# Optimization experiments

Measured on AMD Instinct MI355X. Metric: run time of the kernel, lower is better.

Reference implementation:

```python
import jax, jax.numpy as jnp
import numpy as np

HEADS = 16
DIM_HEAD = 64
SCALE = DIM_HEAD ** -0.5
MASK_VALUE = -jnp.finfo(jnp.float32).max


def setup_inputs() -> dict:
    key = jax.random.key(0)
    ks = jax.random.split(key, 6)
    b, n, dim = 2, 2048, 1024
    mem_len = 2048
    inner = HEADS * DIM_HEAD  # 1024
    return {
        "x": jax.random.normal(ks[0], (b, n, dim), jnp.float32),
        "mem_k": jax.random.normal(ks[1], (b, mem_len, inner), jnp.float32),
        "mem_v": jax.random.normal(ks[2], (b, mem_len, inner), jnp.float32),
        "pos_bias": jax.random.normal(ks[3], (HEADS, n, mem_len + n), jnp.float32) * 0.02,
        "Wq": jax.random.normal(ks[4], (dim, inner), jnp.float32) * (dim ** -0.5),
        "Wkv": jax.random.normal(ks[5], (dim, 2 * inner), jnp.float32) * (dim ** -0.5),
    }


def reference(x, mem_k, mem_v, pos_bias, Wq, Wkv):
    b, n, _ = x.shape
    # projections (note: original module returns before applying to_out)
    q = (x @ Wq) * SCALE                      # [b, n, h*d]
    k, v = jnp.split(x @ Wkv, 2, axis=-1)     # each [b, n, h*d]
    k = jnp.concatenate((mem_k, k), axis=1)   # [b, j, h*d]
    v = jnp.concatenate((mem_v, v), axis=1)

    def split_heads(t):
        return t.reshape(t.shape[0], t.shape[1], HEADS, DIM_HEAD).transpose(0, 2, 1, 3)

    q, k, v = map(split_heads, (q, k, v))     # [b, h, i/j, d]
    sim = jnp.einsum('bhid,bhjd->bhij', q, k)
    sim = sim + pos_bias[None]                # broadcast over batch
    i, j = sim.shape[-2:]
    # causal mask: triu with offset j - i + 1 is masked out
    causal_mask = jnp.triu(jnp.ones((i, j), dtype=bool), k=j - i + 1)
    sim = jnp.where(causal_mask[None, None], MASK_VALUE, sim)
    attn = jax.nn.softmax(sim, axis=-1)
    out = jnp.einsum('bhij,bhjd->bhid', attn, v)     # [b, h, i, d]
    out = out.transpose(0, 2, 1, 3).reshape(b, n, HEADS * DIM_HEAD)
    return out
```

## Files before the change

### kernel.cpp

```cpp
#include <hip/hip_runtime.h>
#include <hip/hip_bf16.h>
#include <cstdint>

#define B_     2
#define N_     2048
#define DIM_   1024
#define H_     16
#define DH_    64
#define MEM_   2048
#define JT_    4096
#define INNER_ 1024
#define SCALE_ 0.125f

typedef float f32x4 __attribute__((ext_vector_type(4)));
typedef short s16x8 __attribute__((ext_vector_type(8)));
typedef short s16x4 __attribute__((ext_vector_type(4)));

__device__ __forceinline__ short bf16_of(float f) {
    __hip_bfloat16 h = __float2bfloat16(f);
    return *(short*)&h;
}

__device__ __forceinline__ void gload16(const void* g, short* l) {
    __builtin_amdgcn_global_load_lds(
        (const __attribute__((address_space(1))) unsigned int*)g,
        (__attribute__((address_space(3))) unsigned int*)l, 16, 0, 0);
}

__global__ __launch_bounds__(256) void cast_x(
    const float* __restrict__ x, short* __restrict__ xb)
{
    const int total4 = B_ * N_ * DIM_ / 4;
    for (int idx = blockIdx.x * blockDim.x + threadIdx.x; idx < total4;
         idx += gridDim.x * blockDim.x) {
        float4 v = ((const float4*)x)[idx];
        s16x4 o;
        o[0] = bf16_of(v.x); o[1] = bf16_of(v.y);
        o[2] = bf16_of(v.z); o[3] = bf16_of(v.w);
        *(s16x4*)&xb[idx * 4] = o;
    }
}

__global__ __launch_bounds__(256) void cast_w(
    const float* __restrict__ Wq, const float* __restrict__ Wkv,
    short* __restrict__ Wt)
{
    const int kt = blockIdx.x;
    const int nt = blockIdx.y;
    __shared__ float tile[64][65];
    const int t = threadIdx.x;
    const int r = t >> 2, s4 = (t & 3) * 16;

    const int n0 = nt * 64;
    const float* src;
    int ldn, nc0;
    if (n0 < 1024) { src = Wq;  ldn = 1024; nc0 = n0; }
    else           { src = Wkv; ldn = 2048; nc0 = n0 - 1024; }
    const float scale = (n0 < 1024) ? SCALE_ : 1.0f;

#pragma unroll
    for (int kq = 0; kq < 4; ++kq) {
        float4 v = *(const float4*)&src[(size_t)(kt * 64 + r) * ldn + nc0 + s4 + kq * 4];
        tile[s4 + kq * 4 + 0][r] = v.x;
        tile[s4 + kq * 4 + 1][r] = v.y;
        tile[s4 + kq * 4 + 2][r] = v.z;
        tile[s4 + kq * 4 + 3][r] = v.w;
    }
    __syncthreads();
    short ov[16];
#pragma unroll
    for (int e = 0; e < 16; ++e) ov[e] = bf16_of(tile[r][s4 + e] * scale);
    short* dst = &Wt[(size_t)(n0 + r) * 1024 + kt * 64 + s4];
    *(s16x8*)&dst[0] = *(s16x8*)&ov[0];
    *(s16x8*)&dst[8] = *(s16x8*)&ov[8];
}

#define PLDC 152

__global__ __launch_bounds__(256) void mfma_proj(
    const short* __restrict__ Wt, const short* __restrict__ xb,
    short* __restrict__ qbuf, short* __restrict__ kbuf, short* __restrict__ vtbuf)
{
    const int bc = blockIdx.x;
    const int bi = blockIdx.y;
    const int tid = threadIdx.x;
    const int w = tid >> 6, lane = tid & 63, g = lane >> 4, li = lane & 15;
    const int wr = w >> 1, wc = w & 1;

    __shared__ short smem[128 * PLDC];
    short* A_lds = smem;
    short* B_lds = smem + 8192;

    f32x4 acc[4][4];
#pragma unroll
    for (int m = 0; m < 4; ++m)
#pragma unroll
        for (int n = 0; n < 4; ++n) acc[m][n] = f32x4{0.f, 0.f, 0.f, 0.f};

    const size_t arow0 = (size_t)bc * 128;
    const size_t brow0 = (size_t)bi * 128;

    for (int t = 0; t < 16; ++t) {
        __syncthreads();
#pragma unroll
        for (int u = 0; u < 4; ++u) {
            const int c = (w * 4 + u) * 64 + lane;
            const int row = c >> 3, q = c & 7;
            const int qs = q ^ (row & 7);
            gload16(&Wt[(arow0 + row) * 1024 + t * 64 + qs * 8],
                    &A_lds[(w * 4 + u) * 512 + lane * 8]);
            gload16(&xb[(brow0 + row) * 1024 + t * 64 + qs * 8],
                    &B_lds[(w * 4 + u) * 512 + lane * 8]);
        }
        __syncthreads();
#pragma unroll
        for (int kc = 0; kc < 2; ++kc) {
            s16x8 af[4], bf[4];
#pragma unroll
            for (int mt = 0; mt < 4; ++mt) {
                const int row = wr * 64 + mt * 16 + li;
                af[mt] = *(const s16x8*)&A_lds[row * 64 + ((kc * 4 + g) ^ (row & 7)) * 8];
            }
#pragma unroll
            for (int nt = 0; nt < 4; ++nt) {
                const int row = wc * 64 + nt * 16 + li;
                bf[nt] = *(const s16x8*)&B_lds[row * 64 + ((kc * 4 + g) ^ (row & 7)) * 8];
            }
#pragma unroll
            for (int mt = 0; mt < 4; ++mt)
#pragma unroll
                for (int nt = 0; nt < 4; ++nt)
                    acc[mt][nt] = __builtin_amdgcn_mfma_f32_16x16x32_bf16(af[mt], bf[nt], acc[mt][nt], 0, 0, 0);
        }
    }

    __syncthreads();
    const int c0 = bc * 128;
    const int i0g = bi * 128;
    const int b = i0g >> 11;
    const int ii0 = i0g & 2047;

    if (c0 < 2048) {
#pragma unroll
        for (int mt = 0; mt < 4; ++mt)
#pragma unroll
            for (int nt = 0; nt < 4; ++nt) {
                const int i_l = wc * 64 + nt * 16 + li;
                const int c_l = wr * 64 + mt * 16 + g * 4;
                s16x4 v4;
                v4[0] = bf16_of(acc[mt][nt][0]);
                v4[1] = bf16_of(acc[mt][nt][1]);
                v4[2] = bf16_of(acc[mt][nt][2]);
                v4[3] = bf16_of(acc[mt][nt][3]);
                *(s16x4*)&smem[i_l * PLDC + c_l] = v4;
            }
        __syncthreads();
        const bool isq = (c0 < 1024);
#pragma unroll
        for (int u = 0; u < 8; ++u) {
            const int ch = tid + u * 256;
            const int i_l = ch >> 4, seg = ch & 15;
            s16x8 v = *(const s16x8*)&smem[i_l * PLDC + seg * 8];
            const int cg = c0 + seg * 8;
            const int h = (cg >> 6) & 15;
            const int d = cg & 63;
            if (isq)
                *(s16x8*)&qbuf[(((size_t)(b * H_ + h)) * N_ + ii0 + i_l) * DH_ + d] = v;
            else
                *(s16x8*)&kbuf[(((size_t)(b * H_ + h)) * JT_ + MEM_ + ii0 + i_l) * DH_ + d] = v;
        }
    } else {
#pragma unroll
        for (int mt = 0; mt < 4; ++mt)
#pragma unroll
            for (int nt = 0; nt < 4; ++nt) {
                const int i_l = wc * 64 + nt * 16 + li;
                const int c_b = wr * 64 + mt * 16 + g * 4;
#pragma unroll
                for (int r = 0; r < 4; ++r)
                    smem[(c_b + r) * PLDC + i_l] = bf16_of(acc[mt][nt][r]);
            }
        __syncthreads();
#pragma unroll
        for (int u = 0; u < 8; ++u) {
            const int ch = tid + u * 256;
            const int c_l = ch >> 4, seg = ch & 15;
            s16x8 v = *(const s16x8*)&smem[c_l * PLDC + seg * 8];
            const int cv = c0 + c_l - 2048;
            const int h = cv >> 6, d = cv & 63;
            *(s16x8*)&vtbuf[(((size_t)(b * H_ + h)) * DH_ + d) * JT_ + MEM_ + ii0 + seg * 8] = v;
        }
    }
}

__global__ __launch_bounds__(256) void copymem_k(
    const float* __restrict__ mem_k, short* __restrict__ kbuf)
{
    const int total4 = B_ * MEM_ * INNER_ / 4;
    for (int idx = blockIdx.x * blockDim.x + threadIdx.x; idx < total4;
         idx += gridDim.x * blockDim.x) {
        const int flat = idx * 4;
        const int c = flat & 1023;
        const int j = (flat >> 10) & 2047;
        const int b = flat >> 21;
        const int h = c >> 6, d = c & 63;
        float4 v = ((const float4*)mem_k)[idx];
        s16x4 o;
        o[0] = bf16_of(v.x); o[1] = bf16_of(v.y);
        o[2] = bf16_of(v.z); o[3] = bf16_of(v.w);
        *(s16x4*)&kbuf[(((size_t)(b * H_ + h)) * JT_ + j) * DH_ + d] = o;
    }
}

__global__ __launch_bounds__(256) void transpose_memv(
    const float* __restrict__ mem_v, short* __restrict__ vtbuf)
{
    const int jt = blockIdx.x, h = blockIdx.y, b = blockIdx.z;
    const int j0 = jt * 64;
    __shared__ float tile[64][65];
    const int t = threadIdx.x;
    const int r = t >> 2, s4 = (t & 3) * 16;
#pragma unroll
    for (int k = 0; k < 4; ++k) {
        float4 v = *(const float4*)&mem_v[((size_t)(b * MEM_ + j0 + r)) * INNER_ + h * DH_ + s4 + k * 4];
        tile[s4 + k * 4 + 0][r] = v.x;
        tile[s4 + k * 4 + 1][r] = v.y;
        tile[s4 + k * 4 + 2][r] = v.z;
        tile[s4 + k * 4 + 3][r] = v.w;
    }
    __syncthreads();
    short ov[16];
#pragma unroll
    for (int e = 0; e < 16; ++e) ov[e] = bf16_of(tile[r][s4 + e]);
    short* dst = &vtbuf[((size_t)((b * H_ + h) * DH_ + r)) * JT_ + j0 + s4];
    *(s16x8*)&dst[0] = *(s16x8*)&ov[0];
    *(s16x8*)&dst[8] = *(s16x8*)&ov[8];
}

#define LPP 72

__global__ __launch_bounds__(256) void attn_flash(
    const short* __restrict__ qbuf, const short* __restrict__ kbuf,
    const short* __restrict__ vtbuf, const float* __restrict__ pos_bias,
    float* __restrict__ out)
{
    const int lid = blockIdx.x;
    const int k_  = lid & 255;
    const int hi  = lid >> 8;
    const int h   = (k_ & 7) | (((k_ >> 3) & 1) << 3);
    const int b   = (k_ >> 4) & 1;
    const int ztl = k_ >> 5;
    const int zt  = hi ? (15 - ztl) : ztl;
    const int i0  = zt * 128;

    const int tid = threadIdx.x;
    const int w = tid >> 6, lane = tid & 63, g = lane >> 4, li = lane & 15;

    __shared__ short K_lds[2][64 * 64];
    __shared__ short VT_lds[2][64 * 64];
    __shared__ short P_lds[4][32 * LPP];

    const size_t bh = b * H_ + h;
    const short* kg  = kbuf  + bh * (size_t)JT_ * DH_;
    const short* vtg = vtbuf + bh * (size_t)DH_ * JT_;
    const float* pb  = pos_bias + (size_t)h * N_ * JT_;

    const int qw = i0 + w * 32;

    s16x8 aq[2][2];
#pragma unroll
    for (int mt = 0; mt < 2; ++mt)
#pragma unroll
        for (int kc = 0; kc < 2; ++kc)
            aq[mt][kc] = *(const s16x8*)&qbuf[(bh * N_ + qw + mt * 16 + li) * DH_ + kc * 32 + g * 8];

    f32x4 o[2][4];
    float m_run[2], l_run[2];
#pragma unroll
    for (int mt = 0; mt < 2; ++mt) {
#pragma unroll
        for (int dt = 0; dt < 4; ++dt) o[mt][dt] = f32x4{0.f, 0.f, 0.f, 0.f};
        m_run[mt] = -3.0e38f; l_run[mt] = 0.f;
    }

    const int ntiles = 34 + 2 * zt;

    #define STAGE(bufi, j0s)                                                   \
    {                                                                          \
        _Pragma("unroll")                                                      \
        for (int u = 0; u < 2; ++u) {                                          \
            const int c = u * 256 + tid;                                       \
            const int row = c >> 3, q = c & 7;                                 \
            const int qs = q ^ (row & 7);                                      \
            gload16(&kg[(size_t)((j0s) + row) * DH_ + qs * 8],                 \
                    &K_lds[bufi][c * 8]);                                      \
            gload16(&vtg[(size_t)row * JT_ + (j0s) + qs * 8],                  \
                    &VT_lds[bufi][c * 8]);                                     \
        }                                                                      \
    }

    f32x4 bnext[2][4];
    #define LOADB(j0s)                                                         \
    {                                                                          \
        _Pragma("unroll")                                                      \
        for (int mt = 0; mt < 2; ++mt)                                         \
        _Pragma("unroll")                                                      \
        for (int nt = 0; nt < 4; ++nt)                                         \
            bnext[mt][nt] = *(const f32x4*)&pb[(size_t)(qw + mt * 16 + li) * JT_ + (j0s) + nt * 16 + g * 4]; \
    }

    STAGE(0, 0);
    LOADB(0);
    __syncthreads();

    for (int t = 0; t < ntiles; ++t) {
        const int cur = t & 1;
        const int j0 = t * 64;

        if (t + 1 < ntiles) STAGE(cur ^ 1, j0 + 64);

        f32x4 sacc[2][4];
#pragma unroll
        for (int mt = 0; mt < 2; ++mt)
#pragma unroll
            for (int nt = 0; nt < 4; ++nt) sacc[mt][nt] = bnext[mt][nt];

        if (t + 1 < ntiles) LOADB(j0 + 64);

        __builtin_amdgcn_s_setprio(1);
#pragma unroll
        for (int kc = 0; kc < 2; ++kc)
#pragma unroll
            for (int nt = 0; nt < 4; ++nt) {
                s16x8 bk = *(const s16x8*)&K_lds[cur][(nt * 16 + li) * 64 + ((kc * 4 + g) ^ (li & 7)) * 8];
                sacc[0][nt] = __builtin_amdgcn_mfma_f32_16x16x32_bf16(bk, aq[0][kc], sacc[0][nt], 0, 0, 0);
                sacc[1][nt] = __builtin_amdgcn_mfma_f32_16x16x32_bf16(bk, aq[1][kc], sacc[1][nt], 0, 0, 0);
            }
        __builtin_amdgcn_s_setprio(0);

#pragma unroll
        for (int mt = 0; mt < 2; ++mt) {
            const int q = qw + mt * 16 + li;
            if (j0 + 63 > MEM_ + qw + mt * 16) {
#pragma unroll
                for (int nt = 0; nt < 4; ++nt)
#pragma unroll
                    for (int r = 0; r < 4; ++r) {
                        const int jg = j0 + nt * 16 + g * 4 + r;
                        if (jg > MEM_ + q) sacc[mt][nt][r] = -1e30f;
                    }
            }
            float t0 = fmaxf(fmaxf(sacc[mt][0][0], sacc[mt][0][1]), fmaxf(sacc[mt][0][2], sacc[mt][0][3]));
            float t1 = fmaxf(fmaxf(sacc[mt][1][0], sacc[mt][1][1]), fmaxf(sacc[mt][1][2], sacc[mt][1][3]));
            float t2 = fmaxf(fmaxf(sacc[mt][2][0], sacc[mt][2][1]), fmaxf(sacc[mt][2][2], sacc[mt][2][3]));
            float t3 = fmaxf(fmaxf(sacc[mt][3][0], sacc[mt][3][1]), fmaxf(sacc[mt][3][2], sacc[mt][3][3]));
            float tm = fmaxf(fmaxf(t0, t1), fmaxf(t2, t3));
            tm = fmaxf(tm, __shfl_xor(tm, 16));
            tm = fmaxf(tm, __shfl_xor(tm, 32));
            const float m_new = fmaxf(m_run[mt], tm);
            const float sc = __expf(m_run[mt] - m_new);
            m_run[mt] = m_new;

#pragma unroll
            for (int nt = 0; nt < 4; ++nt)
#pragma unroll
                for (int r = 0; r < 4; ++r)
                    sacc[mt][nt][r] = __expf(sacc[mt][nt][r] - m_new);

            float s0 = (sacc[mt][0][0] + sacc[mt][0][1]) + (sacc[mt][0][2] + sacc[mt][0][3]);
            float s1 = (sacc[mt][1][0] + sacc[mt][1][1]) + (sacc[mt][1][2] + sacc[mt][1][3]);
            float s2 = (sacc[mt][2][0] + sacc[mt][2][1]) + (sacc[mt][2][2] + sacc[mt][2][3]);
            float s3 = (sacc[mt][3][0] + sacc[mt][3][1]) + (sacc[mt][3][2] + sacc[mt][3][3]);
            float ts = (s0 + s1) + (s2 + s3);
            ts += __shfl_xor(ts, 16);
            ts += __shfl_xor(ts, 32);
            l_run[mt] = l_run[mt] * sc + ts;
#pragma unroll
            for (int dt = 0; dt < 4; ++dt) o[mt][dt] *= sc;

#pragma unroll
            for (int nt = 0; nt < 4; ++nt) {
                s16x4 pk;
                pk[0] = bf16_of(sacc[mt][nt][0]);
                pk[1] = bf16_of(sacc[mt][nt][1]);
                pk[2] = bf16_of(sacc[mt][nt][2]);
                pk[3] = bf16_of(sacc[mt][nt][3]);
                *(s16x4*)&P_lds[w][(mt * 16 + li) * LPP + nt * 16 + g * 4] = pk;
            }
        }

        __builtin_amdgcn_s_setprio(1);
#pragma unroll
        for (int kc = 0; kc < 2; ++kc) {
            s16x8 pf[2];
#pragma unroll
            for (int mt = 0; mt < 2; ++mt) {
                s16x4 plo = *(const s16x4*)&P_lds[w][(mt * 16 + li) * LPP + kc * 32 + g * 8];
                s16x4 phi = *(const s16x4*)&P_lds[w][(mt * 16 + li) * LPP + kc * 32 + g * 8 + 4];
#pragma unroll
                for (int e = 0; e < 4; ++e) { pf[mt][e] = plo[e]; pf[mt][4 + e] = phi[e]; }
            }
#pragma unroll
            for (int dt = 0; dt < 4; ++dt) {
                s16x8 bv = *(const s16x8*)&VT_lds[cur][(dt * 16 + li) * 64 + ((kc * 4 + g) ^ (li & 7)) * 8];
                o[0][dt] = __builtin_amdgcn_mfma_f32_16x16x32_bf16(bv, pf[0], o[0][dt], 0, 0, 0);
                o[1][dt] = __builtin_amdgcn_mfma_f32_16x16x32_bf16(bv, pf[1], o[1][dt], 0, 0, 0);
            }
        }
        __builtin_amdgcn_s_setprio(0);

        __syncthreads();
    }
    #undef STAGE
    #undef LOADB

#pragma unroll
    for (int mt = 0; mt < 2; ++mt) {
        const float rinv = 1.0f / l_run[mt];
        const int q = qw + mt * 16 + li;
#pragma unroll
        for (int dt = 0; dt < 4; ++dt) {
            f32x4 ov = o[mt][dt] * rinv;
            *(f32x4*)&out[((size_t)(b * N_ + q)) * INNER_ + h * DH_ + dt * 16 + g * 4] = ov;
        }
    }
}

extern "C" void kernel_launch(void* const* d_in, const int* in_sizes, int n_in,
                              void* d_out, int out_size, void* d_ws, size_t ws_size,
                              hipStream_t stream)
{
    const float* x        = (const float*)d_in[0];
    const float* mem_k    = (const float*)d_in[1];
    const float* mem_v    = (const float*)d_in[2];
    const float* pos_bias = (const float*)d_in[3];
    const float* Wq       = (const float*)d_in[4];
    const float* Wkv      = (const float*)d_in[5];
    float* out = (float*)d_out;

    char* ws = (char*)d_ws;
    short* qbuf  = (short*)(ws);
    short* kbuf  = (short*)(ws + (8u << 20));
    short* vtbuf = (short*)(ws + (24u << 20));
    short* xb    = (short*)(ws + (40u << 20));
    short* Wt    = (short*)(ws + (48u << 20));

    cast_x<<<2048, 256, 0, stream>>>(x, xb);
    cast_w<<<dim3(16, 48), 256, 0, stream>>>(Wq, Wkv, Wt);
    copymem_k<<<2048, 256, 0, stream>>>(mem_k, kbuf);
    transpose_memv<<<dim3(32, H_, B_), 256, 0, stream>>>(mem_v, vtbuf);

    mfma_proj<<<dim3(24, 32), 256, 0, stream>>>(Wt, xb, qbuf, kbuf, vtbuf);

    attn_flash<<<512, 256, 0, stream>>>(qbuf, kbuf, vtbuf, pos_bias, out);
}
```

Before: 263.6 us.

## Drop LDS staging of K/V and read fragments directly from global memory

Removes the double-buffered LDS staging of K and V^T tiles and has each warp load its MFMA operands straight from global memory (relying on L1/L2). Blocks are remapped so each block covers 64 query rows, with warps split across the two batches and half-tiles of queries, giving finer causal tile counts. This cuts LDS traffic and the block-wide sync, but each warp now issues its own uncoalesced global K/V loads with no sharing across warps, exposing global latency inside the MFMA loop.

```diff
diff --git a/kernel.cpp b/kernel.cpp
--- a/kernel.cpp
+++ b/kernel.cpp
@@ -248,25 +248,22 @@
     const int k_  = lid & 255;
     const int hi  = lid >> 8;
     const int h   = (k_ & 7) | (((k_ >> 3) & 1) << 3);
-    const int b   = (k_ >> 4) & 1;
-    const int ztl = k_ >> 5;
-    const int zt  = hi ? (15 - ztl) : ztl;
-    const int i0  = zt * 128;
+    const int zql = k_ >> 4;
+    const int zq  = hi ? (31 - zql) : zql;
+    const int i0  = zq * 64;
 
     const int tid = threadIdx.x;
     const int w = tid >> 6, lane = tid & 63, g = lane >> 4, li = lane & 15;
-
-    __shared__ short K_lds[2][64 * 64];
-    __shared__ short VT_lds[2][64 * 64];
+    const int b  = w & 1;
+    const int qw = i0 + (w >> 1) * 32;
+
     __shared__ short P_lds[4][32 * LPP];
 
-    const size_t bh = b * H_ + h;
+    const size_t bh = (size_t)(b * H_ + h);
     const short* kg  = kbuf  + bh * (size_t)JT_ * DH_;
     const short* vtg = vtbuf + bh * (size_t)DH_ * JT_;
     const float* pb  = pos_bias + (size_t)h * N_ * JT_;
 
-    const int qw = i0 + w * 32;
-
     s16x8 aq[2][2];
 #pragma unroll
     for (int mt = 0; mt < 2; ++mt)
@@ -283,21 +280,7 @@
         m_run[mt] = -3.0e38f; l_run[mt] = 0.f;
     }
 
-    const int ntiles = 34 + 2 * zt;
-
-    #define STAGE(bufi, j0s)                                                   \
-    {                                                                          \
-        _Pragma("unroll")                                                      \
-        for (int u = 0; u < 2; ++u) {                                          \
-            const int c = u * 256 + tid;                                       \
-            const int row = c >> 3, q = c & 7;                                 \
-            const int qs = q ^ (row & 7);                                      \
-            gload16(&kg[(size_t)((j0s) + row) * DH_ + qs * 8],                 \
-                    &K_lds[bufi][c * 8]);                                      \
-            gload16(&vtg[(size_t)row * JT_ + (j0s) + qs * 8],                  \
-                    &VT_lds[bufi][c * 8]);                                     \
-        }                                                                      \
-    }
+    const int ntiles = 33 + zq;
 
     f32x4 bnext[2][4];
     #define LOADB(j0s)                                                         \
@@ -309,16 +292,13 @@
             bnext[mt][nt] = *(const f32x4*)&pb[(size_t)(qw + mt * 16 + li) * JT_ + (j0s) + nt * 16 + g * 4]; \
     }
 
-    STAGE(0, 0);
     LOADB(0);
-    __syncthreads();
 
     for (int t = 0; t < ntiles; ++t) {
-        const int cur = t & 1;
+        __builtin_amdgcn_s_barrier();
+
         const int j0 = t * 64;
 
-        if (t + 1 < ntiles) STAGE(cur ^ 1, j0 + 64);
-
         f32x4 sacc[2][4];
 #pragma unroll
         for (int mt = 0; mt < 2; ++mt)
@@ -332,7 +312,7 @@
         for (int kc = 0; kc < 2; ++kc)
 #pragma unroll
             for (int nt = 0; nt < 4; ++nt) {
-                s16x8 bk = *(const s16x8*)&K_lds[cur][(nt * 16 + li) * 64 + ((kc * 4 + g) ^ (li & 7)) * 8];
+                s16x8 bk = *(const s16x8*)&kg[(size_t)(j0 + nt * 16 + li) * DH_ + kc * 32 + g * 8];
                 sacc[0][nt] = __builtin_amdgcn_mfma_f32_16x16x32_bf16(bk, aq[0][kc], sacc[0][nt], 0, 0, 0);
                 sacc[1][nt] = __builtin_amdgcn_mfma_f32_16x16x32_bf16(bk, aq[1][kc], sacc[1][nt], 0, 0, 0);
             }
@@ -402,16 +382,13 @@
             }
 #pragma unroll
             for (int dt = 0; dt < 4; ++dt) {
-                s16x8 bv = *(const s16x8*)&VT_lds[cur][(dt * 16 + li) * 64 + ((kc * 4 + g) ^ (li & 7)) * 8];
+                s16x8 bv = *(const s16x8*)&vtg[(size_t)(dt * 16 + li) * JT_ + j0 + kc * 32 + g * 8];
                 o[0][dt] = __builtin_amdgcn_mfma_f32_16x16x32_bf16(bv, pf[0], o[0][dt], 0, 0, 0);
                 o[1][dt] = __builtin_amdgcn_mfma_f32_16x16x32_bf16(bv, pf[1], o[1][dt], 0, 0, 0);
             }
         }
         __builtin_amdgcn_s_setprio(0);
-
-        __syncthreads();
-    }
-    #undef STAGE
+    }
     #undef LOADB
 
 #pragma unroll
```

After: 416.3 us. 57.9% more time.

## Split attention block into 8 waves of 16 query rows each

Applied to the files above, without the earlier changes.

The flash-attention kernel moves from 4 waves each owning 32 query rows to 8 waves each owning 16 rows, launched with 512 threads per block. Each wave now holds half the accumulators and bias registers, and every thread issues one global-to-LDS load per stage instead of two. The aim is more waves in flight to hide the pos_bias global-load latency and the softmax work. In exchange each K/V LDS fragment read feeds only one MFMA instead of two, so LDS traffic per MFMA doubles, and barrier synchronisation now spans more waves.

```diff
diff --git a/kernel.cpp b/kernel.cpp
--- a/kernel.cpp
+++ b/kernel.cpp
@@ -239,7 +239,7 @@
 
 #define LPP 72
 
-__global__ __launch_bounds__(256) void attn_flash(
+__global__ __launch_bounds__(512) void attn_flash(
     const short* __restrict__ qbuf, const short* __restrict__ kbuf,
     const short* __restrict__ vtbuf, const float* __restrict__ pos_bias,
     float* __restrict__ out)
@@ -258,55 +258,44 @@
 
     __shared__ short K_lds[2][64 * 64];
     __shared__ short VT_lds[2][64 * 64];
-    __shared__ short P_lds[4][32 * LPP];
-
-    const size_t bh = b * H_ + h;
+    __shared__ short P_lds[8][16 * LPP];
+
+    const size_t bh = (size_t)(b * H_ + h);
     const short* kg  = kbuf  + bh * (size_t)JT_ * DH_;
     const short* vtg = vtbuf + bh * (size_t)DH_ * JT_;
     const float* pb  = pos_bias + (size_t)h * N_ * JT_;
 
-    const int qw = i0 + w * 32;
-
-    s16x8 aq[2][2];
-#pragma unroll
-    for (int mt = 0; mt < 2; ++mt)
-#pragma unroll
-        for (int kc = 0; kc < 2; ++kc)
-            aq[mt][kc] = *(const s16x8*)&qbuf[(bh * N_ + qw + mt * 16 + li) * DH_ + kc * 32 + g * 8];
-
-    f32x4 o[2][4];
-    float m_run[2], l_run[2];
-#pragma unroll
-    for (int mt = 0; mt < 2; ++mt) {
-#pragma unroll
-        for (int dt = 0; dt < 4; ++dt) o[mt][dt] = f32x4{0.f, 0.f, 0.f, 0.f};
-        m_run[mt] = -3.0e38f; l_run[mt] = 0.f;
-    }
+    const int qw = i0 + w * 16;
+
+    s16x8 aq[2];
+#pragma unroll
+    for (int kc = 0; kc < 2; ++kc)
+        aq[kc] = *(const s16x8*)&qbuf[(bh * N_ + qw + li) * DH_ + kc * 32 + g * 8];
+
+    f32x4 o[4];
+    float m_run = -3.0e38f, l_run = 0.f;
+#pragma unroll
+    for (int dt = 0; dt < 4; ++dt) o[dt] = f32x4{0.f, 0.f, 0.f, 0.f};
 
     const int ntiles = 34 + 2 * zt;
 
     #define STAGE(bufi, j0s)                                                   \
     {                                                                          \
-        _Pragma("unroll")                                                      \
-        for (int u = 0; u < 2; ++u) {                                          \
-            const int c = u * 256 + tid;                                       \
-            const int row = c >> 3, q = c & 7;                                 \
-            const int qs = q ^ (row & 7);                                      \
-            gload16(&kg[(size_t)((j0s) + row) * DH_ + qs * 8],                 \
-                    &K_lds[bufi][c * 8]);                                      \
-            gload16(&vtg[(size_t)row * JT_ + (j0s) + qs * 8],                  \
-                    &VT_lds[bufi][c * 8]);                                     \
-        }                                                                      \
-    }
-
-    f32x4 bnext[2][4];
+        const int c = tid;                                                     \
+        const int row = c >> 3, q = c & 7;                                     \
+        const int qs = q ^ (row & 7);                                          \
+        gload16(&kg[(size_t)((j0s) + row) * DH_ + qs * 8],                     \
+                &K_lds[bufi][c * 8]);                                          \
+        gload16(&vtg[(size_t)row * JT_ + (j0s) + qs * 8],                      \
+                &VT_lds[bufi][c * 8]);                                         \
+    }
+
+    f32x4 bnext[4];
     #define LOADB(j0s)                                                         \
     {                                                                          \
         _Pragma("unroll")                                                      \
-        for (int mt = 0; mt < 2; ++mt)                                         \
-        _Pragma("unroll")                                                      \
         for (int nt = 0; nt < 4; ++nt)                                         \
-            bnext[mt][nt] = *(const f32x4*)&pb[(size_t)(qw + mt * 16 + li) * JT_ + (j0s) + nt * 16 + g * 4]; \
+            bnext[nt] = *(const f32x4*)&pb[(size_t)(qw + li) * JT_ + (j0s) + nt * 16 + g * 4]; \
     }
 
     STAGE(0, 0);
@@ -316,16 +305,15 @@
     for (int t = 0; t < ntiles; ++t) {
         const int cur = t & 1;
         const int j0 = t * 64;
-
-        if (t + 1 < ntiles) STAGE(cur ^ 1, j0 + 64);
-
-        f32x4 sacc[2][4];
-#pragma unroll
-        for (int mt = 0; mt < 2; ++mt)
-#pragma unroll
-            for (int nt = 0; nt < 4; ++nt) sacc[mt][nt] = bnext[mt][nt];
-
-        if (t + 1 < ntiles) LOADB(j0 + 64);
+        const bool more = (t + 1 < ntiles);
+
+        if (more) STAGE(cur ^ 1, j0 + 64);
+
+        f32x4 sacc[4];
+#pragma unroll
+        for (int nt = 0; nt < 4; ++nt) sacc[nt] = bnext[nt];
+
+        if (more) LOADB(j0 + 64);
 
         __builtin_amdgcn_s_setprio(1);
 #pragma unroll
@@ -333,78 +321,67 @@
 #pragma unroll
             for (int nt = 0; nt < 4; ++nt) {
                 s16x8 bk = *(const s16x8*)&K_lds[cur][(nt * 16 + li) * 64 + ((kc * 4 + g) ^ (li & 7)) * 8];
-                sacc[0][nt] = __builtin_amdgcn_mfma_f32_16x16x32_bf16(bk, aq[0][kc], sacc[0][nt], 0, 0, 0);
-                sacc[1][nt] = __builtin_amdgcn_mfma_f32_16x16x32_bf16(bk, aq[1][kc], sacc[1][nt], 0, 0, 0);
+                sacc[nt] = __builtin_amdgcn_mfma_f32_16x16x32_bf16(bk, aq[kc], sacc[nt], 0, 0, 0);
             }
         __builtin_amdgcn_s_setprio(0);
 
-#pragma unroll
-        for (int mt = 0; mt < 2; ++mt) {
-            const int q = qw + mt * 16 + li;
-            if (j0 + 63 > MEM_ + qw + mt * 16) {
-#pragma unroll
-                for (int nt = 0; nt < 4; ++nt)
-#pragma unroll
-                    for (int r = 0; r < 4; ++r) {
-                        const int jg = j0 + nt * 16 + g * 4 + r;
-                        if (jg > MEM_ + q) sacc[mt][nt][r] = -1e30f;
-                    }
-            }
-            float t0 = fmaxf(fmaxf(sacc[mt][0][0], sacc[mt][0][1]), fmaxf(sacc[mt][0][2], sacc[mt][0][3]));
-            float t1 = fmaxf(fmaxf(sacc[mt][1][0], sacc[mt][1][1]), fmaxf(sacc[mt][1][2], sacc[mt][1][3]));
-            float t2 = fmaxf(fmaxf(sacc[mt][2][0], sacc[mt][2][1]), fmaxf(sacc[mt][2][2], sacc[mt][2][3]));
-            float t3 = fmaxf(fmaxf(sacc[mt][3][0], sacc[mt][3][1]), fmaxf(sacc[mt][3][2], sacc[mt][3][3]));
-            float tm = fmaxf(fmaxf(t0, t1), fmaxf(t2, t3));
-            tm = fmaxf(tm, __shfl_xor(tm, 16));
-            tm = fmaxf(tm, __shfl_xor(tm, 32));
-            const float m_new = fmaxf(m_run[mt], tm);
-            const float sc = __expf(m_run[mt] - m_new);
-            m_run[mt] = m_new;
-
+        const int q = qw + li;
+        if (j0 + 63 > MEM_ + qw) {
 #pragma unroll
             for (int nt = 0; nt < 4; ++nt)
 #pragma unroll
-                for (int r = 0; r < 4; ++r)
-                    sacc[mt][nt][r] = __expf(sacc[mt][nt][r] - m_new);
-
-            float s0 = (sacc[mt][0][0] + sacc[mt][0][1]) + (sacc[mt][0][2] + sacc[mt][0][3]);
-            float s1 = (sacc[mt][1][0] + sacc[mt][1][1]) + (sacc[mt][1][2] + sacc[mt][1][3]);
-            float s2 = (sacc[mt][2][0] + sacc[mt][2][1]) + (sacc[mt][2][2] + sacc[mt][2][3]);
-            float s3 = (sacc[mt][3][0] + sacc[mt][3][1]) + (sacc[mt][3][2] + sacc[mt][3][3]);
-            float ts = (s0 + s1) + (s2 + s3);
-            ts += __shfl_xor(ts, 16);
-            ts += __shfl_xor(ts, 32);
-            l_run[mt] = l_run[mt] * sc + ts;
-#pragma unroll
-            for (int dt = 0; dt < 4; ++dt) o[mt][dt] *= sc;
-
-#pragma unroll
-            for (int nt = 0; nt < 4; ++nt) {
-                s16x4 pk;
-                pk[0] = bf16_of(sacc[mt][nt][0]);
-                pk[1] = bf16_of(sacc[mt][nt][1]);
-                pk[2] = bf16_of(sacc[mt][nt][2]);
-                pk[3] = bf16_of(sacc[mt][nt][3]);
-                *(s16x4*)&P_lds[w][(mt * 16 + li) * LPP + nt * 16 + g * 4] = pk;
-            }
+                for (int r = 0; r < 4; ++r) {
+                    const int jg = j0 + nt * 16 + g * 4 + r;
+                    if (jg > MEM_ + q) sacc[nt][r] = -1e30f;
+                }
+        }
+
+        float t0 = fmaxf(fmaxf(sacc[0][0], sacc[0][1]), fmaxf(sacc[0][2], sacc[0][3]));
+        float t1 = fmaxf(fmaxf(sacc[1][0], sacc[1][1]), fmaxf(sacc[1][2], sacc[1][3]));
+        float t2 = fmaxf(fmaxf(sacc[2][0], sacc[2][1]), fmaxf(sacc[2][2], sacc[2][3]));
+        float t3 = fmaxf(fmaxf(sacc[3][0], sacc[3][1]), fmaxf(sacc[3][2], sacc[3][3]));
+        float tm = fmaxf(fmaxf(t0, t1), fmaxf(t2, t3));
+        tm = fmaxf(tm, __shfl_xor(tm, 16));
+        tm = fmaxf(tm, __shfl_xor(tm, 32));
+        const float m_new = fmaxf(m_run, tm);
+        const float sc = __expf(m_run - m_new);
+        m_run = m_new;
+
+#pragma unroll
+        for (int nt = 0; nt < 4; ++nt)
+#pragma unroll
+            for (int r = 0; r < 4; ++r)
+                sacc[nt][r] = __expf(sacc[nt][r] - m_new);
+
+        float s0 = (sacc[0][0] + sacc[0][1]) + (sacc[0][2] + sacc[0][3]);
+        float s1 = (sacc[1][0] + sacc[1][1]) + (sacc[1][2] + sacc[1][3]);
+        float s2 = (sacc[2][0] + sacc[2][1]) + (sacc[2][2] + sacc[2][3]);
+        float s3 = (sacc[3][0] + sacc[3][1]) + (sacc[3][2] + sacc[3][3]);
+        float ts = (s0 + s1) + (s2 + s3);
+        ts += __shfl_xor(ts, 16);
+        ts += __shfl_xor(ts, 32);
+        l_run = l_run * sc + ts;
+#pragma unroll
+        for (int dt = 0; dt < 4; ++dt) o[dt] *= sc;
+
+#pragma unroll
+        for (int nt = 0; nt < 4; ++nt) {
+            s16x4 pk;
+            pk[0] = bf16_of(sacc[nt][0]);
+            pk[1] = bf16_of(sacc[nt][1]);
+            pk[2] = bf16_of(sacc[nt][2]);
+            pk[3] = bf16_of(sacc[nt][3]);
+            *(s16x4*)&P_lds[w][li * LPP + nt * 16 + g * 4] = pk;
         }
 
         __builtin_amdgcn_s_setprio(1);
 #pragma unroll
         for (int kc = 0; kc < 2; ++kc) {
-            s16x8 pf[2];
-#pragma unroll
-            for (int mt = 0; mt < 2; ++mt) {
-                s16x4 plo = *(const s16x4*)&P_lds[w][(mt * 16 + li) * LPP + kc * 32 + g * 8];
-                s16x4 phi = *(const s16x4*)&P_lds[w][(mt * 16 + li) * LPP + kc * 32 + g * 8 + 4];
-#pragma unroll
-                for (int e = 0; e < 4; ++e) { pf[mt][e] = plo[e]; pf[mt][4 + e] = phi[e]; }
-            }
+            s16x8 pf = *(const s16x8*)&P_lds[w][li * LPP + kc * 32 + g * 8];
 #pragma unroll
             for (int dt = 0; dt < 4; ++dt) {
                 s16x8 bv = *(const s16x8*)&VT_lds[cur][(dt * 16 + li) * 64 + ((kc * 4 + g) ^ (li & 7)) * 8];
-                o[0][dt] = __builtin_amdgcn_mfma_f32_16x16x32_bf16(bv, pf[0], o[0][dt], 0, 0, 0);
-                o[1][dt] = __builtin_amdgcn_mfma_f32_16x16x32_bf16(bv, pf[1], o[1][dt], 0, 0, 0);
+                o[dt] = __builtin_amdgcn_mfma_f32_16x16x32_bf16(bv, pf, o[dt], 0, 0, 0);
             }
         }
         __builtin_amdgcn_s_setprio(0);
@@ -414,13 +391,12 @@
     #undef STAGE
     #undef LOADB
 
-#pragma unroll
-    for (int mt = 0; mt < 2; ++mt) {
-        const float rinv = 1.0f / l_run[mt];
-        const int q = qw + mt * 16 + li;
+    {
+        const float rinv = 1.0f / l_run;
+        const int q = qw + li;
 #pragma unroll
         for (int dt = 0; dt < 4; ++dt) {
-            f32x4 ov = o[mt][dt] * rinv;
+            f32x4 ov = o[dt] * rinv;
             *(f32x4*)&out[((size_t)(b * N_ + q)) * INNER_ + h * DH_ + dt * 16 + g * 4] = ov;
         }
     }
@@ -452,5 +428,5 @@
 
     mfma_proj<<<dim3(24, 32), 256, 0, stream>>>(Wt, xb, qbuf, kbuf, vtbuf);
 
-    attn_flash<<<512, 256, 0, stream>>>(qbuf, kbuf, vtbuf, pos_bias, out);
-}
+    attn_flash<<<512, 512, 0, stream>>>(qbuf, kbuf, vtbuf, pos_bias, out);
+}
```

New measurement: 238.7 us. -9.4%, faster.
